# Performance work log

Measured on AMD Instinct MI355X. Metric: run time of the kernel, lower is better.

The kernel has to match this reference:

```python
import jax, jax.numpy as jnp
import numpy as np

N, F_IN, HEADS, F_OUT = 4096, 128, 4, 32
DENSITY = 0.05


def setup_inputs() -> dict:
    key = jax.random.key(0)
    k_x, k_adj, k_w, k_as, k_ad, k_b = jax.random.split(key, 6)
    x = jax.random.normal(k_x, (N, F_IN), dtype=jnp.float32)
    # binary adjacency with self-loops so every row of Tau_sum is nonzero
    adj = (jax.random.uniform(k_adj, (N, N)) < DENSITY).astype(jnp.float32)
    adj = jnp.maximum(adj, jnp.eye(N, dtype=jnp.float32))
    weight = jax.random.normal(k_w, (HEADS * F_OUT, F_IN), dtype=jnp.float32) * 0.1
    att_src = jax.random.normal(k_as, (1, HEADS, F_OUT), dtype=jnp.float32) * 0.1
    att_dst = jax.random.normal(k_ad, (1, HEADS, F_OUT), dtype=jnp.float32) * 0.1
    bias = jax.random.normal(k_b, (HEADS * F_OUT,), dtype=jnp.float32) * 0.1
    return {"x": x, "adj_matrix": adj, "weight": weight,
            "att_src": att_src, "att_dst": att_dst, "bias": bias}


def reference(x, adj_matrix, weight, att_src, att_dst, bias):
    n = x.shape[0]
    heads = att_src.shape[1]
    f_out = weight.shape[0] // heads
    # H' = x W^T, reshaped to [N, heads, F_out]
    h_prime = (x @ weight.T).reshape(n, heads, f_out)
    alpha_src = jnp.sum(h_prime * att_src, axis=-1)  # [N, heads]
    alpha_dst = jnp.sum(h_prime * att_dst, axis=-1)  # [N, heads]
    # C[m, n, h] = alpha_src[n, h] + alpha_dst[m, h]
    C = alpha_src[None, :, :] + alpha_dst[:, None, :]
    adj_t = adj_matrix.T[..., None]                  # [N, N, 1]
    # exp(leaky_relu(C, 0.2)) masked by adjacency
    tau = adj_t * jnp.exp(jnp.maximum(0.2 * C, C))   # [N, N, heads]
    tau_sum = jnp.sum(tau, axis=1, keepdims=True)    # [N, 1, heads]
    att_weights = tau / tau_sum
    # Z[m, h, f] = sum_n (adjT * att)[m, n, h] * H'[n, h, f]
    z = jnp.einsum('mnh,nhf->mhf', adj_t * att_weights, h_prime)
    return z.reshape(n, heads * f_out) + bias
```

## Files before the change

kernel.cpp:

```cpp
#include <hip/hip_runtime.h>
#include <hip/hip_bf16.h>

#define N_NODES 4096
#define F_IN    128
#define HEADS   4
#define FTOT    128
#define NSPLIT  16
#define NRANGE  (N_NODES / NSPLIT)
#define NSTEP   (NRANGE / 64)
#define HPB     512
#define BITB    1024
#define L2E     1.4426950408889634f

typedef __attribute__((ext_vector_type(8)))  short  short8v;
typedef __attribute__((ext_vector_type(16))) float  float16v;

static __device__ __forceinline__ unsigned f2bfu(float f) {
    union { __hip_bfloat16 h; unsigned short u; } cv;
    cv.h = __float2bfloat16(f);
    return (unsigned)cv.u;
}
static __device__ __forceinline__ unsigned cvt_pk_bf16(float lo, float hi) {
    unsigned r;
    asm("v_cvt_pk_bf16_f32 %0, %1, %2" : "=v"(r) : "v"(lo), "v"(hi));
    return r;
}

__global__ __launch_bounds__(256)
void k_pre(const float* __restrict__ x, const float* __restrict__ W,
           const float* __restrict__ att_src, const float* __restrict__ att_dst,
           const float* __restrict__ adj,
           unsigned short* __restrict__ hpt, float* __restrict__ ast,
           float* __restrict__ adt, unsigned* __restrict__ abits)
{
    const int t = threadIdx.x;
    if (blockIdx.x < HPB) {
        __shared__ alignas(16) float    xs[8 * F_IN];
        __shared__ alignas(16) unsigned hs[F_IN * 4];
        __shared__ float ssa[4][8], ssd[4][8];
        const int sub = t >> 7;
        const int tt  = t & 127;
        const int i0  = blockIdx.x * 8;
        reinterpret_cast<float4*>(xs)[t] =
            reinterpret_cast<const float4*>(x + (size_t)i0 * F_IN)[t];
        __syncthreads();

        const float4* W4  = reinterpret_cast<const float4*>(W + tt * F_IN);
        const float4* xs4 = reinterpret_cast<const float4*>(xs + sub * 4 * F_IN);
        float a0 = 0.f, a1 = 0.f, a2 = 0.f, a3 = 0.f;
#pragma unroll
        for (int k = 0; k < F_IN / 4; ++k) {
            const float4 w  = W4[k];
            const float4 v0 = xs4[k], v1 = xs4[32 + k], v2 = xs4[64 + k], v3 = xs4[96 + k];
            a0 = fmaf(w.x, v0.x, a0); a0 = fmaf(w.y, v0.y, a0); a0 = fmaf(w.z, v0.z, a0); a0 = fmaf(w.w, v0.w, a0);
            a1 = fmaf(w.x, v1.x, a1); a1 = fmaf(w.y, v1.y, a1); a1 = fmaf(w.z, v1.z, a1); a1 = fmaf(w.w, v1.w, a1);
            a2 = fmaf(w.x, v2.x, a2); a2 = fmaf(w.y, v2.y, a2); a2 = fmaf(w.z, v2.z, a2); a2 = fmaf(w.w, v2.w, a2);
            a3 = fmaf(w.x, v3.x, a3); a3 = fmaf(w.y, v3.y, a3); a3 = fmaf(w.z, v3.z, a3); a3 = fmaf(w.w, v3.w, a3);
        }
        hs[tt * 4 + sub * 2 + 0] = f2bfu(a0) | (f2bfu(a1) << 16);
        hs[tt * 4 + sub * 2 + 1] = f2bfu(a2) | (f2bfu(a3) << 16);

        const float asv = att_src[tt], adv = att_dst[tt];
        float s0 = a0 * asv, s1 = a1 * asv, s2 = a2 * asv, s3 = a3 * asv;
        float d0 = a0 * adv, d1 = a1 * adv, d2 = a2 * adv, d3 = a3 * adv;
#pragma unroll
        for (int s = 16; s; s >>= 1) {
            s0 += __shfl_xor(s0, s); s1 += __shfl_xor(s1, s);
            s2 += __shfl_xor(s2, s); s3 += __shfl_xor(s3, s);
            d0 += __shfl_xor(d0, s); d1 += __shfl_xor(d1, s);
            d2 += __shfl_xor(d2, s); d3 += __shfl_xor(d3, s);
        }
        if ((tt & 31) == 0) {
            const int hh = tt >> 5;
            ssa[hh][sub * 4 + 0] = s0 * L2E; ssa[hh][sub * 4 + 1] = s1 * L2E;
            ssa[hh][sub * 4 + 2] = s2 * L2E; ssa[hh][sub * 4 + 3] = s3 * L2E;
            ssd[hh][sub * 4 + 0] = d0 * L2E; ssd[hh][sub * 4 + 1] = d1 * L2E;
            ssd[hh][sub * 4 + 2] = d2 * L2E; ssd[hh][sub * 4 + 3] = d3 * L2E;
        }
        __syncthreads();
        if (t < 128)
            *reinterpret_cast<uint4*>(hpt + (size_t)t * N_NODES + i0) =
                *reinterpret_cast<const uint4*>(&hs[t * 4]);
        if (t < 64) {
            const int sd = t >> 5, hh = (t >> 3) & 3, nn = t & 7;
            const float v = sd ? ssd[hh][nn] : ssa[hh][nn];
            (sd ? adt : ast)[hh * N_NODES + i0 + nn] = v;
        }
    } else {
        __shared__ alignas(16) unsigned short lb[64 * 16];
        const int sblk  = blockIdx.x - HPB;
        const int strip = sblk & 63;
        const int chunk = sblk >> 6;
        const int c0    = strip * 64;
        const int r0    = chunk * 256;
        const int q     = t & 15;
        const int p     = t >> 4;
        const float4* adj4 = reinterpret_cast<const float4*>(adj);

        float4 v[16];
#pragma unroll
        for (int it = 0; it < 16; ++it)
            v[it] = adj4[(size_t)(r0 + p * 16 + it) * (N_NODES / 4) + (c0 >> 2) + q];
        unsigned mk0 = 0, mk1 = 0, mk2 = 0, mk3 = 0;
#pragma unroll
        for (int it = 0; it < 16; ++it) {
            mk0 |= (v[it].x != 0.f) ? (1u << it) : 0u;
            mk1 |= (v[it].y != 0.f) ? (1u << it) : 0u;
            mk2 |= (v[it].z != 0.f) ? (1u << it) : 0u;
            mk3 |= (v[it].w != 0.f) ? (1u << it) : 0u;
        }
        lb[(4 * q + 0) * 16 + p] = (unsigned short)mk0;
        lb[(4 * q + 1) * 16 + p] = (unsigned short)mk1;
        lb[(4 * q + 2) * 16 + p] = (unsigned short)mk2;
        lb[(4 * q + 3) * 16 + p] = (unsigned short)mk3;
        __syncthreads();
        const unsigned* lb32 = reinterpret_cast<const unsigned*>(lb);
#pragma unroll
        for (int j = 0; j < 2; ++j) {
            const int w = t + j * 256;
            const int m = w >> 3, col = w & 7;
            abits[(size_t)(c0 + m) * (N_NODES / 32) + chunk * 8 + col] = lb32[w];
        }
    }
}

__global__ __launch_bounds__(256, 8)
void k_main(const unsigned short* __restrict__ hpt, const float* __restrict__ ast,
            const float* __restrict__ adt, const unsigned* __restrict__ abits,
            unsigned short* __restrict__ zp16, float* __restrict__ taup)
{
    __shared__ alignas(16) float2 ea_s[HEADS * NRANGE];
    const int t     = threadIdx.x;
    const int wv    = t >> 6;
    const int l     = t & 63;
    const int np    = l >> 5;
    const int lm    = l & 31;
    const int mt    = blockIdx.x >> 4;
    const int split = blockIdx.x & 15;
    const int m0    = mt * 32;
    const int nb0   = split * NRANGE;

#pragma unroll
    for (int j = 0; j < 4; ++j) {
        const int lin = j * 256 + t;
        const int h   = lin >> 8;
        const int n   = lin & 255;
        const float a = ast[h * N_NODES + nb0 + n];
        ea_s[lin] = make_float2(__builtin_amdgcn_exp2f(a),
                                __builtin_amdgcn_exp2f(0.2f * a));
    }
    uint4 brow[2];
    {
        const uint4* bsrc = reinterpret_cast<const uint4*>(
            abits + (size_t)(m0 + lm) * (N_NODES / 32) + split * 8);
        brow[0] = bsrc[0];
        brow[1] = bsrc[1];
    }
    const float adm = adt[wv * N_NODES + m0 + lm];
    const float ed1 = __builtin_amdgcn_exp2f(adm);
    const float ed2 = __builtin_amdgcn_exp2f(0.2f * adm);
    __syncthreads();

    const unsigned short* hrow = hpt + (size_t)(wv * 32 + lm) * N_NODES + nb0 + np * 8;
    const float2* eaw = ea_s + wv * NRANGE;

    float16v acc;
#pragma unroll
    for (int r = 0; r < 16; ++r) acc[r] = 0.f;
    float tau = 0.f;

#pragma unroll
    for (int step = 0; step < NSTEP; ++step) {
#pragma unroll
        for (int q = 0; q < 4; ++q) {
            const short8v bv = *reinterpret_cast<const short8v*>(hrow + step * 64 + q * 16);
            const float2* eap = eaw + step * 64 + q * 16 + np * 8;
            const unsigned w32 = (&brow[0].x)[(step * 2 + (q >> 1)) & 7];
            const unsigned bb  = (w32 >> (((q & 1) << 4) + (np << 3))) & 0xFFu;
            float w[8];
#pragma unroll
            for (int i = 0; i < 8; ++i) {
                const float2 e = eap[i];
                const float sel = fmaxf(e.x * ed1, e.y * ed2);
                w[i] = (bb & (1u << i)) ? sel : 0.f;
            }
            const float t01 = w[0] + w[1], t23 = w[2] + w[3];
            const float t45 = w[4] + w[5], t67 = w[6] + w[7];
            tau += (t01 + t23) + (t45 + t67);
            union { short8v v; unsigned u[4]; } af;
            af.u[0] = cvt_pk_bf16(w[0], w[1]);
            af.u[1] = cvt_pk_bf16(w[2], w[3]);
            af.u[2] = cvt_pk_bf16(w[4], w[5]);
            af.u[3] = cvt_pk_bf16(w[6], w[7]);
            acc = __builtin_amdgcn_mfma_f32_32x32x16_bf16(af.v, bv, acc, 0, 0, 0);
        }
    }

    tau += __shfl_xor(tau, 32);
    if (np == 0)
        taup[((size_t)split * HEADS + wv) * N_NODES + m0 + lm] = tau;
    unsigned short* zp = zp16 + (size_t)split * N_NODES * FTOT;
#pragma unroll
    for (int r = 0; r < 16; ++r) {
        const int row = (r & 3) + 8 * (r >> 2) + 4 * np;
        zp[(size_t)(m0 + row) * FTOT + wv * 32 + lm] = (unsigned short)f2bfu(acc[r]);
    }
}

__global__ __launch_bounds__(256)
void k_fin(const unsigned* __restrict__ zp32, const float* __restrict__ taup,
           const float* __restrict__ bias, float* __restrict__ out)
{
    const int idx = blockIdx.x * 256 + threadIdx.x;
    const int m = idx >> 5, f4 = idx & 31, h = f4 >> 3;
    float4 z = make_float4(0.f, 0.f, 0.f, 0.f);
    float ts = 0.f;
#pragma unroll
    for (int s = 0; s < NSPLIT; ++s) {
        const uint2 u = reinterpret_cast<const uint2*>(zp32)[(size_t)s * (N_NODES * FTOT / 4) + idx];
        z.x += __uint_as_float(u.x << 16);
        z.y += __uint_as_float(u.x & 0xffff0000u);
        z.z += __uint_as_float(u.y << 16);
        z.w += __uint_as_float(u.y & 0xffff0000u);
        ts += taup[((size_t)s * HEADS + h) * N_NODES + m];
    }
    const float inv = 1.f / ts;
    const float4 b = reinterpret_cast<const float4*>(bias)[f4];
    float4 o;
    o.x = z.x * inv + b.x; o.y = z.y * inv + b.y;
    o.z = z.z * inv + b.z; o.w = z.w * inv + b.w;
    reinterpret_cast<float4*>(out)[idx] = o;
}

extern "C" void kernel_launch(void* const* d_in, const int* in_sizes, int n_in,
                              void* d_out, int out_size, void* d_ws, size_t ws_size,
                              hipStream_t stream) {
    const float* x       = (const float*)d_in[0];
    const float* adj     = (const float*)d_in[1];
    const float* weight  = (const float*)d_in[2];
    const float* att_src = (const float*)d_in[3];
    const float* att_dst = (const float*)d_in[4];
    const float* bias    = (const float*)d_in[5];
    float* out = (float*)d_out;

    unsigned short* hpt = (unsigned short*)d_ws;
    float* ast = (float*)(hpt + (size_t)FTOT * N_NODES);
    float* adt = ast + (size_t)HEADS * N_NODES;
    unsigned* abits = (unsigned*)(adt + (size_t)HEADS * N_NODES);
    unsigned short* zp16 = (unsigned short*)(abits + (size_t)N_NODES * (N_NODES / 32));
    float* taup = (float*)(zp16 + (size_t)NSPLIT * N_NODES * FTOT);

    k_pre <<<HPB + BITB, 256, 0, stream>>>(x, weight, att_src, att_dst, adj,
                                           hpt, ast, adt, abits);
    k_main<<<(N_NODES / 32) * NSPLIT, 256, 0, stream>>>(hpt, ast, adt, abits,
                                                        zp16, taup);
    k_fin <<<N_NODES * (FTOT / 4) / 256, 256, 0, stream>>>((const unsigned*)zp16,
                                                           taup, bias, out);
}
```

Before: 50.11 us.

## Tile H' in 16-node blocks, halve node splits, vectorize LDS exp reads

```diff
diff --git a/kernel.cpp b/kernel.cpp
--- a/kernel.cpp
+++ b/kernel.cpp
@@ -5,7 +5,7 @@
 #define F_IN    128
 #define HEADS   4
 #define FTOT    128
-#define NSPLIT  16
+#define NSPLIT  8
 #define NRANGE  (N_NODES / NSPLIT)
 #define NSTEP   (NRANGE / 64)
 #define HPB     512
@@ -25,6 +25,7 @@
     asm("v_cvt_pk_bf16_f32 %0, %1, %2" : "=v"(r) : "v"(lo), "v"(hi));
     return r;
 }
+
 
 __global__ __launch_bounds__(256)
 void k_pre(const float* __restrict__ x, const float* __restrict__ W,
@@ -79,7 +80,8 @@
         }
         __syncthreads();
         if (t < 128)
-            *reinterpret_cast<uint4*>(hpt + (size_t)t * N_NODES + i0) =
+            *reinterpret_cast<uint4*>(
+                hpt + ((size_t)(i0 >> 4) * 128 + t) * 16 + (i0 & 15)) =
                 *reinterpret_cast<const uint4*>(&hs[t * 4]);
         if (t < 64) {
             const int sd = t >> 5, hh = (t >> 3) & 3, nn = t & 7;
@@ -124,7 +126,7 @@
     }
 }
 
-__global__ __launch_bounds__(256, 8)
+__global__ __launch_bounds__(256, 4)
 void k_main(const unsigned short* __restrict__ hpt, const float* __restrict__ ast,
             const float* __restrict__ adt, const unsigned* __restrict__ abits,
             unsigned short* __restrict__ zp16, float* __restrict__ taup)
@@ -135,33 +137,33 @@
     const int l     = t & 63;
     const int np    = l >> 5;
     const int lm    = l & 31;
-    const int mt    = blockIdx.x >> 4;
-    const int split = blockIdx.x & 15;
+    const int mt    = blockIdx.x >> 3;
+    const int split = blockIdx.x & 7;
     const int m0    = mt * 32;
     const int nb0   = split * NRANGE;
 
 #pragma unroll
-    for (int j = 0; j < 4; ++j) {
+    for (int j = 0; j < 8; ++j) {
         const int lin = j * 256 + t;
-        const int h   = lin >> 8;
-        const int n   = lin & 255;
+        const int h   = lin >> 9;
+        const int n   = lin & 511;
         const float a = ast[h * N_NODES + nb0 + n];
         ea_s[lin] = make_float2(__builtin_amdgcn_exp2f(a),
                                 __builtin_amdgcn_exp2f(0.2f * a));
     }
-    uint4 brow[2];
+    uint4 brow[4];
     {
         const uint4* bsrc = reinterpret_cast<const uint4*>(
-            abits + (size_t)(m0 + lm) * (N_NODES / 32) + split * 8);
-        brow[0] = bsrc[0];
-        brow[1] = bsrc[1];
+            abits + (size_t)(m0 + lm) * (N_NODES / 32) + split * 16);
+#pragma unroll
+        for (int j = 0; j < 4; ++j) brow[j] = bsrc[j];
     }
     const float adm = adt[wv * N_NODES + m0 + lm];
     const float ed1 = __builtin_amdgcn_exp2f(adm);
     const float ed2 = __builtin_amdgcn_exp2f(0.2f * adm);
     __syncthreads();
 
-    const unsigned short* hrow = hpt + (size_t)(wv * 32 + lm) * N_NODES + nb0 + np * 8;
+    const unsigned short* hbase = hpt + ((size_t)(nb0 >> 4) * 128 + wv * 32 + lm) * 16 + np * 8;
     const float2* eaw = ea_s + wv * NRANGE;
 
     float16v acc;
@@ -173,20 +175,23 @@
     for (int step = 0; step < NSTEP; ++step) {
 #pragma unroll
         for (int q = 0; q < 4; ++q) {
-            const short8v bv = *reinterpret_cast<const short8v*>(hrow + step * 64 + q * 16);
-            const float2* eap = eaw + step * 64 + q * 16 + np * 8;
-            const unsigned w32 = (&brow[0].x)[(step * 2 + (q >> 1)) & 7];
+            const int nq = step * 64 + q * 16;
+            const short8v bv = *reinterpret_cast<const short8v*>(
+                hbase + (size_t)(step * 4 + q) * 2048);
+            const float4* ea4 = reinterpret_cast<const float4*>(eaw + nq) + np * 4;
+            float4 ep0 = ea4[0], ep1 = ea4[1], ep2 = ea4[2], ep3 = ea4[3];
+            const unsigned w32 = (&brow[0].x)[(step * 2 + (q >> 1)) & 15];
             const unsigned bb  = (w32 >> (((q & 1) << 4) + (np << 3))) & 0xFFu;
             float w[8];
-#pragma unroll
-            for (int i = 0; i < 8; ++i) {
-                const float2 e = eap[i];
-                const float sel = fmaxf(e.x * ed1, e.y * ed2);
-                w[i] = (bb & (1u << i)) ? sel : 0.f;
-            }
-            const float t01 = w[0] + w[1], t23 = w[2] + w[3];
-            const float t45 = w[4] + w[5], t67 = w[6] + w[7];
-            tau += (t01 + t23) + (t45 + t67);
+            w[0] = (bb & 1u)   ? fmaxf(ep0.x * ed1, ep0.y * ed2) : 0.f;
+            w[1] = (bb & 2u)   ? fmaxf(ep0.z * ed1, ep0.w * ed2) : 0.f;
+            w[2] = (bb & 4u)   ? fmaxf(ep1.x * ed1, ep1.y * ed2) : 0.f;
+            w[3] = (bb & 8u)   ? fmaxf(ep1.z * ed1, ep1.w * ed2) : 0.f;
+            w[4] = (bb & 16u)  ? fmaxf(ep2.x * ed1, ep2.y * ed2) : 0.f;
+            w[5] = (bb & 32u)  ? fmaxf(ep2.z * ed1, ep2.w * ed2) : 0.f;
+            w[6] = (bb & 64u)  ? fmaxf(ep3.x * ed1, ep3.y * ed2) : 0.f;
+            w[7] = (bb & 128u) ? fmaxf(ep3.z * ed1, ep3.w * ed2) : 0.f;
+            tau += ((w[0] + w[1]) + (w[2] + w[3])) + ((w[4] + w[5]) + (w[6] + w[7]));
             union { short8v v; unsigned u[4]; } af;
             af.u[0] = cvt_pk_bf16(w[0], w[1]);
             af.u[1] = cvt_pk_bf16(w[2], w[3]);
```

Measured after the change: 88.18 us. 1.76x slower.
